# Kernel tuning notes

Measured on AMD Instinct MI355X. Metric: run time of the kernel, lower is better.

## Reference

```python
import jax, jax.numpy as jnp
import numpy as np

B, T, E, U, V = 4096, 80, 100, 64, 10000

def setup_inputs() -> dict:
    key = jax.random.key(0)
    ks = jax.random.split(key, 10)
    s = lambda *sh: 0.05
    return {
        "tokens": jax.random.randint(ks[0], (B, T), 0, V, dtype=jnp.int32),
        "emb": jax.random.normal(ks[1], (V, E), jnp.float32) * 0.05,
        "k0": jax.random.normal(ks[2], (E, 4 * U), jnp.float32) * 0.05,
        "r0": jax.random.normal(ks[3], (U, 4 * U), jnp.float32) * 0.05,
        "b0": jnp.zeros((4 * U,), jnp.float32),
        "k1": jax.random.normal(ks[4], (E, 4 * U), jnp.float32) * 0.05,
        "r1": jax.random.normal(ks[5], (U, 4 * U), jnp.float32) * 0.05,
        "b1": jnp.zeros((4 * U,), jnp.float32),
        "Wd": jax.random.normal(ks[6], (U, 1), jnp.float32) * 0.05,
        "bd": jnp.zeros((1,), jnp.float32),
    }

def _lstm_cell(h, c, xt, k, r, b):
    # keras LSTMCell gate order: i, f, g(cell candidate), o
    z = xt @ k + h @ r + b  # [B, 4U]
    i, f, g, o = jnp.split(z, 4, axis=-1)
    c_new = jax.nn.sigmoid(f) * c + jax.nn.sigmoid(i) * jnp.tanh(g)
    h_new = jax.nn.sigmoid(o) * jnp.tanh(c_new)
    return h_new, c_new

def reference(tokens, emb, k0, r0, b0, k1, r1, b1, Wd, bd):
    x = emb[tokens]                 # [B, T, E]
    xs = jnp.swapaxes(x, 0, 1)      # [T, B, E] for scan over time
    zeros = jnp.zeros((tokens.shape[0], U), x.dtype)
    init = (zeros, zeros, zeros, zeros)  # h0, c0, h1, c1

    def step(state, xt):
        h0, c0, h1, c1 = state
        h0, c0 = _lstm_cell(h0, c0, xt, k0, r0, b0)
        # NOTE: original feeds the raw embedded word (not out0) to cell 1
        h1, c1 = _lstm_cell(h1, c1, xt, k1, r1, b1)
        return (h0, c0, h1, c1), None

    (h0, c0, h1, c1), _ = jax.lax.scan(step, init, xs)
    logits = h1 @ Wd + bd           # [B, 1]
    return jax.nn.sigmoid(logits)
```

## Files before the change

kernel.cpp:

```cpp
#include <hip/hip_runtime.h>
#include <hip/hip_bf16.h>

#define B_  4096
#define T_  80
#define E_  100
#define U_  64
#define G_  256
#define V_  10000

#define S_H  72
#define AS   136

typedef __attribute__((ext_vector_type(8))) __bf16 bf16x8;
typedef __attribute__((ext_vector_type(4))) __bf16 bf16x4;
typedef __attribute__((ext_vector_type(4))) float  floatx4;

__device__ __forceinline__ float sigmoidf_(float x) {
    return __fdividef(1.f, 1.f + __expf(-x));
}

__device__ __forceinline__ float tanhf_(float x) {
    return 1.f - __fdividef(2.f, __expf(2.f * x) + 1.f);
}

__global__ __launch_bounds__(256) void embk_kernel(const float* __restrict__ emb,
                                                   const float* __restrict__ k1,
                                                   const float* __restrict__ b1,
                                                   float* __restrict__ embk) {
    __shared__ __bf16 aLDS[64 * AS];

    const int tid  = threadIdx.x;
    const int lane = tid & 63;
    const int w    = tid >> 6;
    const int n    = lane & 15;
    const int kg   = lane >> 4;
    const int v0   = (blockIdx.x >> 1) * 64;
    const int n0   = (blockIdx.x & 1) * 128;
    const int nrows = min(64, V_ - v0);

    for (int i = tid; i < 64 * AS / 8; i += 256) {
        bf16x8 z;
#pragma unroll
        for (int jj = 0; jj < 8; ++jj) z[jj] = (__bf16)0.f;
        *(bf16x8*)(aLDS + i * 8) = z;
    }

    bf16x8 bfr[2][4];
#pragma unroll
    for (int ct = 0; ct < 2; ++ct)
#pragma unroll
        for (int kc = 0; kc < 4; ++kc) {
            bf16x8 s;
#pragma unroll
            for (int jj = 0; jj < 8; ++jj) {
                int k = kc * 32 + kg * 8 + jj;
                s[jj] = (k < E_) ? (__bf16)k1[k * G_ + n0 + w * 32 + ct * 16 + n]
                                 : (__bf16)0.f;
            }
            bfr[ct][kc] = s;
        }
    const float bv0 = b1[n0 + w * 32 + n];
    const float bv1 = b1[n0 + w * 32 + 16 + n];

    __syncthreads();

    for (int i = tid; i < nrows * 25; i += 256) {
        int r = i / 25, q = i - r * 25;
        float4 ev = *(const float4*)(emb + (long)(v0 + r) * E_ + q * 4);
        bf16x4 bv; bv[0] = (__bf16)ev.x; bv[1] = (__bf16)ev.y;
                   bv[2] = (__bf16)ev.z; bv[3] = (__bf16)ev.w;
        *(bf16x4*)(aLDS + r * AS + q * 4) = bv;
    }
    __syncthreads();

#pragma unroll
    for (int mt = 0; mt < 4; ++mt) {
        const __bf16* ab = aLDS + (mt * 16 + n) * AS + kg * 8;
        bf16x8 a0 = *(const bf16x8*)(ab + 0);
        bf16x8 a1 = *(const bf16x8*)(ab + 32);
        bf16x8 a2 = *(const bf16x8*)(ab + 64);
        bf16x8 a3 = *(const bf16x8*)(ab + 96);
#pragma unroll
        for (int ct = 0; ct < 2; ++ct) {
            float bv = ct ? bv1 : bv0;
            floatx4 acc = {bv, bv, bv, bv};
            acc = __builtin_amdgcn_mfma_f32_16x16x32_bf16(a0, bfr[ct][0], acc, 0, 0, 0);
            acc = __builtin_amdgcn_mfma_f32_16x16x32_bf16(a1, bfr[ct][1], acc, 0, 0, 0);
            acc = __builtin_amdgcn_mfma_f32_16x16x32_bf16(a2, bfr[ct][2], acc, 0, 0, 0);
            acc = __builtin_amdgcn_mfma_f32_16x16x32_bf16(a3, bfr[ct][3], acc, 0, 0, 0);
#pragma unroll
            for (int r = 0; r < 4; ++r) {
                int v = v0 + mt * 16 + kg * 4 + r;
                if (v < V_) embk[(long)v * G_ + n0 + w * 32 + ct * 16 + n] = acc[r];
            }
        }
    }
}

__global__ __launch_bounds__(256) void lstm_kernel(const int*   __restrict__ tokens,
                                                   const float* __restrict__ embk,
                                                   const float* __restrict__ r1,
                                                   const float* __restrict__ Wd,
                                                   const float* __restrict__ bd,
                                                   float* __restrict__ out) {
    __shared__ int    tokLDS[16 * T_];
    __shared__ __bf16 hbuf[2][16 * S_H];

    const int tid  = threadIdx.x;
    const int lane = tid & 63;
    const int w    = tid >> 6;
    const int n    = lane & 15;
    const int kg   = lane >> 4;
    const int bb   = blockIdx.x * 16;

    for (int i = tid; i < 16 * T_; i += 256) tokLDS[i] = tokens[bb * T_ + i];
    for (int i = tid; i < 2 * 16 * S_H; i += 256) (&hbuf[0][0])[i] = (__bf16)0.f;

    bf16x8 afr[4][2];
#pragma unroll
    for (int ct = 0; ct < 4; ++ct)
#pragma unroll
        for (int kc = 0; kc < 2; ++kc) {
            bf16x8 s;
#pragma unroll
            for (int jj = 0; jj < 8; ++jj)
                s[jj] = (__bf16)r1[(kc * 32 + kg * 8 + jj) * G_ + ct * 64 + w * 16 + n];
            afr[ct][kc] = s;
        }

    float c[4] = {0.f, 0.f, 0.f, 0.f};

    __syncthreads();

    floatx4 xkb[2][4];
#pragma unroll
    for (int s = 0; s < 2; ++s) {
        const float* base = embk + (long)tokLDS[n * T_ + s] * G_ + w * 16 + kg * 4;
#pragma unroll
        for (int ct = 0; ct < 4; ++ct)
            xkb[s][ct] = *(const floatx4*)(base + ct * 64);
    }

    auto step = [&](int t, int sel) {
        const __bf16* hb = hbuf[sel ^ 1];
        bf16x8 b0 = *(const bf16x8*)(hb + n * S_H + kg * 8);
        bf16x8 b1 = *(const bf16x8*)(hb + n * S_H + 32 + kg * 8);

        floatx4 acc[4];
#pragma unroll
        for (int ct = 0; ct < 4; ++ct) {
            floatx4 a = xkb[sel][ct];
            a = __builtin_amdgcn_mfma_f32_16x16x32_bf16(afr[ct][0], b0, a, 0, 0, 0);
            a = __builtin_amdgcn_mfma_f32_16x16x32_bf16(afr[ct][1], b1, a, 0, 0, 0);
            acc[ct] = a;
        }

        if (t + 2 < T_) {
            const float* base = embk + (long)tokLDS[n * T_ + t + 2] * G_ + w * 16 + kg * 4;
#pragma unroll
            for (int ct = 0; ct < 4; ++ct)
                xkb[sel][ct] = *(const floatx4*)(base + ct * 64);
        }

        bf16x4 hv;
#pragma unroll
        for (int r = 0; r < 4; ++r) {
            float zi = acc[0][r], zf = acc[1][r], zg = acc[2][r], zo = acc[3][r];
            float cn = sigmoidf_(zf) * c[r] + sigmoidf_(zi) * tanhf_(zg);
            float hn = sigmoidf_(zo) * tanhf_(cn);
            c[r] = cn;
            hv[r] = (__bf16)hn;
        }
        *(bf16x4*)(&hbuf[sel][0] + n * S_H + w * 16 + kg * 4) = hv;

        __syncthreads();
    };

    for (int t = 0; t < T_; t += 2) {
        step(t,     0);
        step(t + 1, 1);
    }

    if (tid < 16) {
        const __bf16* hb = hbuf[1] + tid * S_H;
        float s = bd[0];
#pragma unroll
        for (int u = 0; u < U_; ++u) s = fmaf((float)hb[u], Wd[u], s);
        out[bb + tid] = sigmoidf_(s);
    }
}

extern "C" void kernel_launch(void* const* d_in, const int* in_sizes, int n_in,
                              void* d_out, int out_size, void* d_ws, size_t ws_size,
                              hipStream_t stream) {
    const int*   tokens = (const int*)  d_in[0];
    const float* emb    = (const float*)d_in[1];
    const float* k1     = (const float*)d_in[5];
    const float* r1     = (const float*)d_in[6];
    const float* b1     = (const float*)d_in[7];
    const float* Wd     = (const float*)d_in[8];
    const float* bd     = (const float*)d_in[9];
    float*       out    = (float*)d_out;

    float* embk = (float*)d_ws;

    embk_kernel<<<((V_ + 63) / 64) * 2, 256, 0, stream>>>(emb, k1, b1, embk);
    lstm_kernel<<<B_ / 16, 256, 0, stream>>>(tokens, embk, r1, Wd, bd, out);
}
```

Before: 159.6 us.

## Load embedding rows directly into MFMA fragments and use lightweight LDS barrier

The embedding-projection kernel now handles 16 vocabulary rows per block and loads each row straight from global memory into bf16 MFMA A-fragments in registers. This removes the LDS zero-fill, the staging copy and two block barriers, and launches four times more blocks. The LSTM recurrence replaces __syncthreads with an inline s_waitcnt lgkmcnt(0) plus s_barrier, so the barrier waits only on LDS traffic and not on the outstanding global prefetches of the next step's embk rows. The handwritten barrier depends on the compiler not reordering memory operations around the asm, and the register-loaded bfr weights are now reloaded by four times as many blocks.

```diff
diff --git a/kernel.cpp b/kernel.cpp
--- a/kernel.cpp
+++ b/kernel.cpp
@@ -9,7 +9,6 @@
 #define V_  10000
 
 #define S_H  72
-#define AS   136
 
 typedef __attribute__((ext_vector_type(8))) __bf16 bf16x8;
 typedef __attribute__((ext_vector_type(4))) __bf16 bf16x4;
@@ -21,28 +20,44 @@
 
 __device__ __forceinline__ float tanhf_(float x) {
     return 1.f - __fdividef(2.f, __expf(2.f * x) + 1.f);
+}
+
+__device__ __forceinline__ void lds_barrier_() {
+    asm volatile("s_waitcnt lgkmcnt(0)\n\ts_barrier" ::: "memory");
 }
 
 __global__ __launch_bounds__(256) void embk_kernel(const float* __restrict__ emb,
                                                    const float* __restrict__ k1,
                                                    const float* __restrict__ b1,
                                                    float* __restrict__ embk) {
-    __shared__ __bf16 aLDS[64 * AS];
-
     const int tid  = threadIdx.x;
     const int lane = tid & 63;
     const int w    = tid >> 6;
     const int n    = lane & 15;
     const int kg   = lane >> 4;
-    const int v0   = (blockIdx.x >> 1) * 64;
+    const int v0   = (blockIdx.x >> 1) * 16;
     const int n0   = (blockIdx.x & 1) * 128;
-    const int nrows = min(64, V_ - v0);
-
-    for (int i = tid; i < 64 * AS / 8; i += 256) {
-        bf16x8 z;
-#pragma unroll
-        for (int jj = 0; jj < 8; ++jj) z[jj] = (__bf16)0.f;
-        *(bf16x8*)(aLDS + i * 8) = z;
+
+    const float* erow = emb + (long)(v0 + n) * E_ + kg * 8;
+    bf16x8 afr[4];
+#pragma unroll
+    for (int kc = 0; kc < 3; ++kc) {
+        float4 e0 = *(const float4*)(erow + kc * 32);
+        float4 e1 = *(const float4*)(erow + kc * 32 + 4);
+        bf16x8 s;
+        s[0] = (__bf16)e0.x; s[1] = (__bf16)e0.y; s[2] = (__bf16)e0.z; s[3] = (__bf16)e0.w;
+        s[4] = (__bf16)e1.x; s[5] = (__bf16)e1.y; s[6] = (__bf16)e1.z; s[7] = (__bf16)e1.w;
+        afr[kc] = s;
+    }
+    {
+        bf16x8 s;
+#pragma unroll
+        for (int jj = 0; jj < 8; ++jj) s[jj] = (__bf16)0.f;
+        if (kg == 0) {
+            float4 e0 = *(const float4*)(erow + 96);
+            s[0] = (__bf16)e0.x; s[1] = (__bf16)e0.y; s[2] = (__bf16)e0.z; s[3] = (__bf16)e0.w;
+        }
+        afr[3] = s;
     }
 
     bf16x8 bfr[2][4];
@@ -59,41 +74,18 @@
             }
             bfr[ct][kc] = s;
         }
-    const float bv0 = b1[n0 + w * 32 + n];
-    const float bv1 = b1[n0 + w * 32 + 16 + n];
-
-    __syncthreads();
-
-    for (int i = tid; i < nrows * 25; i += 256) {
-        int r = i / 25, q = i - r * 25;
-        float4 ev = *(const float4*)(emb + (long)(v0 + r) * E_ + q * 4);
-        bf16x4 bv; bv[0] = (__bf16)ev.x; bv[1] = (__bf16)ev.y;
-                   bv[2] = (__bf16)ev.z; bv[3] = (__bf16)ev.w;
-        *(bf16x4*)(aLDS + r * AS + q * 4) = bv;
-    }
-    __syncthreads();
-
-#pragma unroll
-    for (int mt = 0; mt < 4; ++mt) {
-        const __bf16* ab = aLDS + (mt * 16 + n) * AS + kg * 8;
-        bf16x8 a0 = *(const bf16x8*)(ab + 0);
-        bf16x8 a1 = *(const bf16x8*)(ab + 32);
-        bf16x8 a2 = *(const bf16x8*)(ab + 64);
-        bf16x8 a3 = *(const bf16x8*)(ab + 96);
-#pragma unroll
-        for (int ct = 0; ct < 2; ++ct) {
-            float bv = ct ? bv1 : bv0;
-            floatx4 acc = {bv, bv, bv, bv};
-            acc = __builtin_amdgcn_mfma_f32_16x16x32_bf16(a0, bfr[ct][0], acc, 0, 0, 0);
-            acc = __builtin_amdgcn_mfma_f32_16x16x32_bf16(a1, bfr[ct][1], acc, 0, 0, 0);
-            acc = __builtin_amdgcn_mfma_f32_16x16x32_bf16(a2, bfr[ct][2], acc, 0, 0, 0);
-            acc = __builtin_amdgcn_mfma_f32_16x16x32_bf16(a3, bfr[ct][3], acc, 0, 0, 0);
-#pragma unroll
-            for (int r = 0; r < 4; ++r) {
-                int v = v0 + mt * 16 + kg * 4 + r;
-                if (v < V_) embk[(long)v * G_ + n0 + w * 32 + ct * 16 + n] = acc[r];
-            }
-        }
+
+#pragma unroll
+    for (int ct = 0; ct < 2; ++ct) {
+        float bv = b1[n0 + w * 32 + ct * 16 + n];
+        floatx4 acc = {bv, bv, bv, bv};
+        acc = __builtin_amdgcn_mfma_f32_16x16x32_bf16(afr[0], bfr[ct][0], acc, 0, 0, 0);
+        acc = __builtin_amdgcn_mfma_f32_16x16x32_bf16(afr[1], bfr[ct][1], acc, 0, 0, 0);
+        acc = __builtin_amdgcn_mfma_f32_16x16x32_bf16(afr[2], bfr[ct][2], acc, 0, 0, 0);
+        acc = __builtin_amdgcn_mfma_f32_16x16x32_bf16(afr[3], bfr[ct][3], acc, 0, 0, 0);
+#pragma unroll
+        for (int r = 0; r < 4; ++r)
+            embk[(long)(v0 + kg * 4 + r) * G_ + n0 + w * 32 + ct * 16 + n] = acc[r];
     }
 }
 
@@ -173,7 +165,7 @@
         }
         *(bf16x4*)(&hbuf[sel][0] + n * S_H + w * 16 + kg * 4) = hv;
 
-        __syncthreads();
+        lds_barrier_();
     };
 
     for (int t = 0; t < T_; t += 2) {
@@ -204,6 +196,6 @@
 
     float* embk = (float*)d_ws;
 
-    embk_kernel<<<((V_ + 63) / 64) * 2, 256, 0, stream>>>(emb, k1, b1, embk);
+    embk_kernel<<<(V_ / 16) * 2, 256, 0, stream>>>(emb, k1, b1, embk);
     lstm_kernel<<<B_ / 16, 256, 0, stream>>>(tokens, embk, r1, Wd, bd, out);
 }
```

Measured after the change: 161.1 us. No clear change (+0.9%).
